# Performance work log

Measured on AMD Instinct MI355X. Metric: run time of the kernel, lower is better.

The kernel has to match this reference:

```python
import jax, jax.numpy as jnp
import numpy as np

N_U, N_P, E, E_LAB = 100000, 50000, 2000000, 500000
D_U, D_P, H = 64, 128, 64


def _seg_mean(feat, idx, n):
    # scatter-mean: sum per destination / clamp(count, 1)
    s = jax.ops.segment_sum(feat, idx, num_segments=n)
    c = jax.ops.segment_sum(jnp.ones((idx.shape[0],), feat.dtype), idx, num_segments=n)
    return s / jnp.maximum(c, 1.0)[:, None]


def setup_inputs() -> dict:
    key = jax.random.key(0)
    ks = jax.random.split(key, 16)
    inp = {
        'x_user': jax.random.normal(ks[0], (N_U, D_U), jnp.float32),
        'x_product': jax.random.normal(ks[1], (N_P, D_P), jnp.float32),
        'W1_buys_l': jax.random.normal(ks[2], (D_U, H), jnp.float32) * 0.05,
        'b1_buys': jnp.zeros((H,), jnp.float32),
        'W1_buys_r': jax.random.normal(ks[3], (D_P, H), jnp.float32) * 0.05,
        'W1_rev_l': jax.random.normal(ks[4], (D_P, H), jnp.float32) * 0.05,
        'b1_rev': jnp.zeros((H,), jnp.float32),
        'W1_rev_r': jax.random.normal(ks[5], (D_U, H), jnp.float32) * 0.05,
        'W2_buys_l': jax.random.normal(ks[6], (H, H), jnp.float32) * 0.05,
        'b2_buys': jnp.zeros((H,), jnp.float32),
        'W2_buys_r': jax.random.normal(ks[7], (H, H), jnp.float32) * 0.05,
        'W2_rev_l': jax.random.normal(ks[8], (H, H), jnp.float32) * 0.05,
        'b2_rev': jnp.zeros((H,), jnp.float32),
        'W2_rev_r': jax.random.normal(ks[9], (H, H), jnp.float32) * 0.05,
        'edge_src': jax.random.randint(ks[10], (E,), 0, N_U, jnp.int32),
        'edge_dst': jax.random.randint(ks[11], (E,), 0, N_P, jnp.int32),
        'lab_u': jax.random.randint(ks[12], (E_LAB,), 0, N_U, jnp.int32),
        'lab_p': jax.random.randint(ks[13], (E_LAB,), 0, N_P, jnp.int32),
    }
    return inp


def reference(x_user, x_product, W1_buys_l, b1_buys, W1_buys_r, W1_rev_l, b1_rev, W1_rev_r,
              W2_buys_l, b2_buys, W2_buys_r, W2_rev_l, b2_rev, W2_rev_r,
              edge_src, edge_dst, lab_u, lab_p):
    # SAGEConv (mean aggr): out_dst = mean_agg(x_src) @ W_l + b + x_dst @ W_r
    def sage(x_src, x_dst, src, dst, n_dst, Wl, b, Wr):
        agg = _seg_mean(x_src[src], dst, n_dst)
        return agg @ Wl + b + x_dst @ Wr

    n_u, n_p = x_user.shape[0], x_product.shape[0]
    # layer 1 (per edge type, hetero) + relu
    h_p = jax.nn.relu(sage(x_user, x_product, edge_src, edge_dst, n_p, W1_buys_l, b1_buys, W1_buys_r))
    h_u = jax.nn.relu(sage(x_product, x_user, edge_dst, edge_src, n_u, W1_rev_l, b1_rev, W1_rev_r))
    # layer 2
    h_p2 = sage(h_u, h_p, edge_src, edge_dst, n_p, W2_buys_l, b2_buys, W2_buys_r)
    h_u2 = sage(h_p, h_u, edge_dst, edge_src, n_u, W2_rev_l, b2_rev, W2_rev_r)
    # classifier: per-label-edge dot product
    return jnp.sum(h_u2[lab_u] * h_p2[lab_p], axis=-1)
```

## Files before the change

kernel.cpp:

```cpp
#include <hip/hip_runtime.h>


using u16 = unsigned short;
using u32 = unsigned int;

__device__ __forceinline__ u16 bf16r(float f) {
    u32 b = __float_as_uint(f);
    b += 0x7fffu + ((b >> 16) & 1u);
    return (u16)(b >> 16);
}
__device__ __forceinline__ float bflo(u32 u) { return __uint_as_float(u << 16); }
__device__ __forceinline__ float bfhi(u32 u) { return __uint_as_float(u & 0xffff0000u); }

#define BSH 8
#define MAXB 512
#define CHUNK 4096
#define RPT 16

__global__ __launch_bounds__(256) void k_histA(const int* __restrict__ esrc,
                                               const int* __restrict__ edst,
                                               int* __restrict__ bcntP,
                                               int* __restrict__ bcntU,
                                               int NBP, int NBU, int E) {
    __shared__ int hP[MAXB];
    __shared__ int hU[MAXB];
    int tid = threadIdx.x;
    for (int i = tid; i < MAXB; i += 256) { hP[i] = 0; hU[i] = 0; }
    __syncthreads();
    int E4 = E >> 2;
    const int4* s4 = (const int4*)esrc;
    const int4* d4 = (const int4*)edst;
    int stride = gridDim.x * 256;
    for (int i = blockIdx.x * 256 + tid; i < E4; i += stride) {
        int4 s = s4[i], d = d4[i];
        atomicAdd(&hU[s.x >> BSH], 1); atomicAdd(&hU[s.y >> BSH], 1);
        atomicAdd(&hU[s.z >> BSH], 1); atomicAdd(&hU[s.w >> BSH], 1);
        atomicAdd(&hP[d.x >> BSH], 1); atomicAdd(&hP[d.y >> BSH], 1);
        atomicAdd(&hP[d.z >> BSH], 1); atomicAdd(&hP[d.w >> BSH], 1);
    }
    if (blockIdx.x == 0 && tid < (E & 3)) {
        int e = E4 * 4 + tid;
        atomicAdd(&hU[esrc[e] >> BSH], 1);
        atomicAdd(&hP[edst[e] >> BSH], 1);
    }
    __syncthreads();
    for (int i = tid; i < NBP; i += 256) if (hP[i]) atomicAdd(&bcntP[i], hP[i]);
    for (int i = tid; i < NBU; i += 256) if (hU[i]) atomicAdd(&bcntU[i], hU[i]);
}

__global__ __launch_bounds__(256) void k_scanBuckets(const int* __restrict__ cntP,
                                                     int* __restrict__ basesP,
                                                     int* __restrict__ curP, int NBP,
                                                     const int* __restrict__ cntU,
                                                     int* __restrict__ basesU,
                                                     int* __restrict__ curU, int NBU) {
    const int* cnt; int* bases; int* cur; int NB;
    if (blockIdx.x == 0) { cnt = cntP; bases = basesP; cur = curP; NB = NBP; }
    else                 { cnt = cntU; bases = basesU; cur = curU; NB = NBU; }
    __shared__ int sA[MAXB];
    __shared__ int sB[MAXB];
    int tid = threadIdx.x;
    int v0 = (tid < NB) ? cnt[tid] : 0;
    int v1 = (tid + 256 < NB) ? cnt[tid + 256] : 0;
    sA[tid] = v0; sA[tid + 256] = v1;
    __syncthreads();
    int* src = sA; int* dst = sB;
    for (int off = 1; off < MAXB; off <<= 1) {
        dst[tid] = src[tid] + ((tid >= off) ? src[tid - off] : 0);
        int i2 = tid + 256;
        dst[i2] = src[i2] + ((i2 >= off) ? src[i2 - off] : 0);
        __syncthreads();
        int* t = src; src = dst; dst = t;
    }
    if (tid < NB)       { bases[tid] = src[tid] - v0;             cur[tid] = src[tid] - v0; }
    if (tid + 256 < NB) { bases[tid + 256] = src[tid + 256] - v1; cur[tid + 256] = src[tid + 256] - v1; }
    if (tid == 0) bases[NB] = src[MAXB - 1];
}

__global__ __launch_bounds__(256) void k_partition(const int* __restrict__ keys,
                                                   const int* __restrict__ payload,
                                                   int* __restrict__ cursor,
                                                   uint2* __restrict__ pairs,
                                                   int NB, int E) {
    __shared__ int hist[MAXB];
    __shared__ int sA[MAXB];
    __shared__ int sB[MAXB];
    __shared__ int bx[MAXB];
    __shared__ int gbase[MAXB];
    __shared__ uint2 prs[CHUNK];
    int tid = threadIdx.x;
    int i0 = blockIdx.x * CHUNK;
    int count = min(CHUNK, E - i0);
    for (int i = tid; i < MAXB; i += 256) hist[i] = 0;
    __syncthreads();
    int keyr[RPT], payr[RPT], rankr[RPT];
#pragma unroll
    for (int r = 0; r < RPT; ++r) {
        int idx = r * 256 + tid;
        if (idx < count) {
            int k = keys[i0 + idx];
            keyr[r] = k;
            payr[r] = payload[i0 + idx];
            rankr[r] = atomicAdd(&hist[k >> BSH], 1);
        } else keyr[r] = -1;
    }
    __syncthreads();
    sA[tid] = hist[tid]; sA[tid + 256] = hist[tid + 256];
    __syncthreads();
    int* src = sA; int* dst = sB;
    for (int off = 1; off < MAXB; off <<= 1) {
        dst[tid] = src[tid] + ((tid >= off) ? src[tid - off] : 0);
        int i2 = tid + 256;
        dst[i2] = src[i2] + ((i2 >= off) ? src[i2 - off] : 0);
        __syncthreads();
        int* t = src; src = dst; dst = t;
    }
    bx[tid] = src[tid] - hist[tid];
    bx[tid + 256] = src[tid + 256] - hist[tid + 256];
    __syncthreads();
    for (int b = tid; b < NB; b += 256) {
        int c = hist[b];
        gbase[b] = c ? atomicAdd(&cursor[b], c) : 0;
    }
#pragma unroll
    for (int r = 0; r < RPT; ++r) {
        if (keyr[r] >= 0)
            prs[bx[keyr[r] >> BSH] + rankr[r]] = make_uint2((u32)keyr[r], (u32)payr[r]);
    }
    __syncthreads();
    for (int j = tid; j < count; j += 256) {
        uint2 pr = prs[j];
        int b = pr.x >> BSH;
        pairs[gbase[b] + (j - bx[b])] = pr;
    }
}

__global__ __launch_bounds__(256) void k_bucketFill(
    const uint2* __restrict__ pairsP, const int* __restrict__ basesP, int NBP,
    int* __restrict__ nbr_p, int* __restrict__ deg_p, int* __restrict__ ptr_p, int NP,
    const uint2* __restrict__ pairsU, const int* __restrict__ basesU, int NBU,
    int* __restrict__ nbr_u, int* __restrict__ deg_u, int* __restrict__ ptr_u, int NU) {
    const uint2* pairs; const int* bases; int* nbr; int* deg; int* ptr; int N; int bucket;
    if ((int)blockIdx.x < NBP) {
        pairs = pairsP; bases = basesP; nbr = nbr_p; deg = deg_p; ptr = ptr_p; N = NP;
        bucket = blockIdx.x;
    } else {
        pairs = pairsU; bases = basesU; nbr = nbr_u; deg = deg_u; ptr = ptr_u; N = NU;
        bucket = blockIdx.x - NBP;
    }
    int tid = threadIdx.x;
    int base = bases[bucket];
    int cnt = bases[bucket + 1] - base;
    __shared__ int h[256];
    __shared__ int s[256];
    __shared__ int cur[256];
    h[tid] = 0;
    __syncthreads();
    for (int j = tid; j < cnt; j += 256) atomicAdd(&h[pairs[base + j].x & 255], 1);
    __syncthreads();
    int d = h[tid];
    s[tid] = d;
    __syncthreads();
    for (int off = 1; off < 256; off <<= 1) {
        int v = (tid >= off) ? s[tid - off] : 0;
        __syncthreads();
        s[tid] += v;
        __syncthreads();
    }
    int excl = s[tid] - d;
    int node = bucket * 256 + tid;
    if (node < N) { deg[node] = d; ptr[node] = base + excl; }
    cur[tid] = excl;
    __syncthreads();
    for (int j = tid; j < cnt; j += 256) {
        uint2 pr = pairs[base + j];
        int pos = atomicAdd(&cur[pr.x & 255], 1);
        nbr[base + pos] = pr.y;
    }
}

__global__ __launch_bounds__(256) void k_cast8(const float* __restrict__ x,
                                               u16* __restrict__ y, int n8) {
    int i = blockIdx.x * 256 + threadIdx.x;
    if (i >= n8) return;
    const float4* x4 = (const float4*)x;
    float4 a = x4[i * 2], b = x4[i * 2 + 1];
    uint4 o;
    o.x = (u32)bf16r(a.x) | ((u32)bf16r(a.y) << 16);
    o.y = (u32)bf16r(a.z) | ((u32)bf16r(a.w) << 16);
    o.z = (u32)bf16r(b.x) | ((u32)bf16r(b.y) << 16);
    o.w = (u32)bf16r(b.z) | ((u32)bf16r(b.w) << 16);
    ((uint4*)y)[i] = o;
}

__global__ __launch_bounds__(256) void k_transform_bf128(const float* __restrict__ x,
                                                         const float* __restrict__ W,
                                                         u16* __restrict__ ybf, int N) {
    __shared__ float Ws[128 * 64];
    __shared__ float xs[4][128];
    const int tid = threadIdx.x;
    for (int i = tid; i < 128 * 64; i += 256) Ws[i] = W[i];
    const int r = tid >> 6, c = tid & 63;
    const int row0 = blockIdx.x * 4;
    for (int i = tid; i < 4 * 128; i += 256) {
        int rr = i >> 7, kk = i & 127;
        int row = row0 + rr;
        xs[rr][kk] = (row < N) ? x[row * 128 + kk] : 0.f;
    }
    __syncthreads();
    const int row = row0 + r;
    if (row >= N) return;
    float acc = 0.f;
#pragma unroll 8
    for (int k = 0; k < 128; ++k) acc += xs[r][k] * Ws[k * 64 + c];
    ybf[row * 64 + c] = bf16r(acc);
}

__global__ __launch_bounds__(256) void k_gather2(
    const u16* __restrict__ yA, const int* __restrict__ nbrA, const int* __restrict__ startA,
    const int* __restrict__ degA, float* __restrict__ aggA, int NA,
    const u16* __restrict__ yB, const int* __restrict__ nbrB, const int* __restrict__ startB,
    const int* __restrict__ degB, float* __restrict__ aggB, int NB) {
    int w = (blockIdx.x * 256 + threadIdx.x) >> 6;
    int lane = threadIdx.x & 63;
    if (w >= NA + NB) return;
    const u16* y; const int* nbr; const int* stp; const int* deg; float* agg; int n;
    if (w < NA) { y = yA; nbr = nbrA; stp = startA; deg = degA; agg = aggA; n = w; }
    else        { y = yB; nbr = nbrB; stp = startB; deg = degB; agg = aggB; n = w - NA; }
    const int q = lane >> 3, t = lane & 7;
    const int d = deg[n];
    int j = stp[n];
    const int end = j + d;
    float a0=0,a1=0,a2=0,a3=0,a4=0,a5=0,a6=0,a7=0;
    float b0=0,b1=0,b2=0,b3=0,b4=0,b5=0,b6=0,b7=0;
    for (; j + 16 <= end; j += 16) {
        int g0 = nbr[j + q], g1 = nbr[j + 8 + q];
        uint4 v0 = *(const uint4*)(y + g0 * 64 + t * 8);
        uint4 v1 = *(const uint4*)(y + g1 * 64 + t * 8);
        a0 += bflo(v0.x); a1 += bfhi(v0.x); a2 += bflo(v0.y); a3 += bfhi(v0.y);
        a4 += bflo(v0.z); a5 += bfhi(v0.z); a6 += bflo(v0.w); a7 += bfhi(v0.w);
        b0 += bflo(v1.x); b1 += bfhi(v1.x); b2 += bflo(v1.y); b3 += bfhi(v1.y);
        b4 += bflo(v1.z); b5 += bfhi(v1.z); b6 += bflo(v1.w); b7 += bfhi(v1.w);
    }
    for (; j + 8 <= end; j += 8) {
        int g0 = nbr[j + q];
        uint4 v0 = *(const uint4*)(y + g0 * 64 + t * 8);
        a0 += bflo(v0.x); a1 += bfhi(v0.x); a2 += bflo(v0.y); a3 += bfhi(v0.y);
        a4 += bflo(v0.z); a5 += bfhi(v0.z); a6 += bflo(v0.w); a7 += bfhi(v0.w);
    }
    if (j + q < end) {
        int g0 = nbr[j + q];
        uint4 v0 = *(const uint4*)(y + g0 * 64 + t * 8);
        a0 += bflo(v0.x); a1 += bfhi(v0.x); a2 += bflo(v0.y); a3 += bfhi(v0.y);
        a4 += bflo(v0.z); a5 += bfhi(v0.z); a6 += bflo(v0.w); a7 += bfhi(v0.w);
    }
    a0 += b0; a1 += b1; a2 += b2; a3 += b3; a4 += b4; a5 += b5; a6 += b6; a7 += b7;
#pragma unroll
    for (int m = 8; m < 64; m <<= 1) {
        a0 += __shfl_xor(a0, m, 64); a1 += __shfl_xor(a1, m, 64);
        a2 += __shfl_xor(a2, m, 64); a3 += __shfl_xor(a3, m, 64);
        a4 += __shfl_xor(a4, m, 64); a5 += __shfl_xor(a5, m, 64);
        a6 += __shfl_xor(a6, m, 64); a7 += __shfl_xor(a7, m, 64);
    }
    if (q == 0) {
        float dinv = 1.0f / (float)max(d, 1);
        float* dstp = agg + n * 64 + t * 8;
        float4 o0, o1;
        o0.x = a0 * dinv; o0.y = a1 * dinv; o0.z = a2 * dinv; o0.w = a3 * dinv;
        o1.x = a4 * dinv; o1.y = a5 * dinv; o1.z = a6 * dinv; o1.w = a7 * dinv;
        *(float4*)dstp = o0;
        *(float4*)(dstp + 4) = o1;
    }
}

#define FMA_ROW(ACC, O, W4) \
    ACC[0] += (O) * (W4).x; ACC[1] += (O) * (W4).y; \
    ACC[2] += (O) * (W4).z; ACC[3] += (O) * (W4).w;

template <int K, int ROWS, bool RELU, bool EMIT, bool PRE, bool BIAS>
__global__ __launch_bounds__(256) void k_ctile(const float* __restrict__ pre,
                                               const float* __restrict__ bias,
                                               const float* __restrict__ x,
                                               const float* __restrict__ W,
                                               float* __restrict__ h,
                                               u16* __restrict__ hbf, int N) {
    constexpr int RR = ROWS / 16;
    constexpr int STRIDE = K + 4;
    constexpr int KF4 = K / 4;
    __shared__ float Ws[K * 64];
    __shared__ float op[ROWS * STRIDE];
    const int tid = threadIdx.x;
    for (int i = tid; i < K * 16; i += 256)
        ((float4*)Ws)[i] = ((const float4*)W)[i];
    const int c4 = (tid & 15) * 4;
    const int rb = (tid >> 4) * RR;
    float bx_ = 0.f, by_ = 0.f, bz_ = 0.f, bw_ = 0.f;
    if (BIAS) {
        float4 b4 = *(const float4*)(bias + c4);
        bx_ = b4.x; by_ = b4.y; bz_ = b4.z; bw_ = b4.w;
    }
    const int ntiles = (N + ROWS - 1) / ROWS;
    for (int tile = blockIdx.x; tile < ntiles; tile += gridDim.x) {
        const int row0 = tile * ROWS;
        __syncthreads();
        for (int i = tid; i < ROWS * KF4; i += 256) {
            int r = i / KF4, k4 = (i % KF4) * 4;
            int row = row0 + r;
            float4 v = make_float4(0.f, 0.f, 0.f, 0.f);
            if (row < N) v = *(const float4*)(x + (size_t)row * K + k4);
            *(float4*)(op + r * STRIDE + k4) = v;
        }
        __syncthreads();
        float acc[RR][4];
#pragma unroll
        for (int i = 0; i < RR; ++i) {
            float px = 0.f, py = 0.f, pz = 0.f, pw = 0.f;
            if (PRE) {
                int row = row0 + rb + i;
                if (row < N) {
                    float4 p = *(const float4*)(pre + row * 64 + c4);
                    px = p.x; py = p.y; pz = p.z; pw = p.w;
                }
            }
            acc[i][0] = bx_ + px; acc[i][1] = by_ + py;
            acc[i][2] = bz_ + pz; acc[i][3] = bw_ + pw;
        }
        for (int kk = 0; kk < K; kk += 4) {
            float4 w0 = *(const float4*)(Ws + (kk + 0) * 64 + c4);
            float4 w1 = *(const float4*)(Ws + (kk + 1) * 64 + c4);
            float4 w2 = *(const float4*)(Ws + (kk + 2) * 64 + c4);
            float4 w3 = *(const float4*)(Ws + (kk + 3) * 64 + c4);
#pragma unroll
            for (int i = 0; i < RR; ++i) {
                float4 o = *(const float4*)(op + (rb + i) * STRIDE + kk);
                FMA_ROW(acc[i], o.x, w0);
                FMA_ROW(acc[i], o.y, w1);
                FMA_ROW(acc[i], o.z, w2);
                FMA_ROW(acc[i], o.w, w3);
            }
        }
#pragma unroll
        for (int i = 0; i < RR; ++i) {
            int row = row0 + rb + i;
            if (row >= N) continue;
            float v0 = acc[i][0], v1 = acc[i][1], v2 = acc[i][2], v3 = acc[i][3];
            if (RELU) {
                v0 = fmaxf(v0, 0.f); v1 = fmaxf(v1, 0.f);
                v2 = fmaxf(v2, 0.f); v3 = fmaxf(v3, 0.f);
            }
            *(float4*)(h + row * 64 + c4) = make_float4(v0, v1, v2, v3);
            if (EMIT) {
                uint2 o;
                o.x = (u32)bf16r(v0) | ((u32)bf16r(v1) << 16);
                o.y = (u32)bf16r(v2) | ((u32)bf16r(v3) << 16);
                *(uint2*)(hbf + row * 64 + c4) = o;
            }
        }
    }
}

__global__ __launch_bounds__(256) void k_classify4(const float* __restrict__ hu,
                                                   const float* __restrict__ hp,
                                                   const int* __restrict__ lu,
                                                   const int* __restrict__ lp,
                                                   float* __restrict__ out, int EL) {
    int w = (blockIdx.x * 256 + threadIdx.x) >> 6;
    int lane = threadIdx.x & 63;
    int q = lane >> 4, t = lane & 15;
    int e = w * 4 + q;
    float v = 0.f;
    if (e < EL) {
        int u = lu[e], p = lp[e];
        float4 a = *(const float4*)(hu + u * 64 + t * 4);
        float4 b = *(const float4*)(hp + p * 64 + t * 4);
        v = a.x * b.x + a.y * b.y + a.z * b.z + a.w * b.w;
    }
#pragma unroll
    for (int m = 1; m < 16; m <<= 1) v += __shfl_xor(v, m, 64);
    if (t == 0 && e < EL) out[e] = v;
}

extern "C" void kernel_launch(void* const* d_in, const int* in_sizes, int n_in,
                              void* d_out, int out_size, void* d_ws, size_t ws_size,
                              hipStream_t stream) {
    const float* x_user    = (const float*)d_in[0];
    const float* x_product = (const float*)d_in[1];
    const float* W1bl = (const float*)d_in[2];
    const float* b1b  = (const float*)d_in[3];
    const float* W1br = (const float*)d_in[4];
    const float* W1rl = (const float*)d_in[5];
    const float* b1r  = (const float*)d_in[6];
    const float* W1rr = (const float*)d_in[7];
    const float* W2bl = (const float*)d_in[8];
    const float* b2b  = (const float*)d_in[9];
    const float* W2br = (const float*)d_in[10];
    const float* W2rl = (const float*)d_in[11];
    const float* b2r  = (const float*)d_in[12];
    const float* W2rr = (const float*)d_in[13];
    const int* esrc = (const int*)d_in[14];
    const int* edst = (const int*)d_in[15];
    const int* lu   = (const int*)d_in[16];
    const int* lp   = (const int*)d_in[17];

    const int NU = in_sizes[0] / 64;
    const int NP = in_sizes[1] / 128;
    const int E  = in_sizes[14];
    const int EL = in_sizes[16];
    const int NBP = (NP + 255) >> BSH;
    const int NBU = (NU + 255) >> BSH;

    char* ws = (char*)d_ws;
    size_t off = 0;
    auto alloc = [&](size_t bytes) -> void* {
        void* p = ws + off;
        off += (bytes + 255) & ~(size_t)255;
        return p;
    };
    int*   deg_u  = (int*)alloc((size_t)NU * 4);
    int*   deg_p  = (int*)alloc((size_t)NP * 4);
    int*   ptr_u  = (int*)alloc((size_t)NU * 4);
    int*   ptr_p  = (int*)alloc((size_t)NP * 4);
    int*   bcntP  = (int*)alloc((size_t)MAXB * 4);
    int*   bcntU  = (int*)alloc((size_t)MAXB * 4);
    int*   basesP = (int*)alloc((size_t)(MAXB + 1) * 4);
    int*   basesU = (int*)alloc((size_t)(MAXB + 1) * 4);
    int*   curP   = (int*)alloc((size_t)MAXB * 4);
    int*   curU   = (int*)alloc((size_t)MAXB * 4);
    int*   nbr_u  = (int*)alloc((size_t)E * 4);
    int*   nbr_p  = (int*)alloc((size_t)E * 4);
    size_t aggBytes = (size_t)(NP + NU) * 64 * 4;
    size_t pairBytes = (size_t)E * 8 * 2;
    char* uni = (char*)alloc(aggBytes > pairBytes ? aggBytes : pairBytes);
    float* aggP   = (float*)uni;
    float* aggU   = (float*)(uni + (size_t)NP * 64 * 4);
    uint2* pairsP = (uint2*)uni;
    uint2* pairsU = (uint2*)(uni + (size_t)E * 8);
    u16*   bfA    = (u16*)alloc((size_t)NU * 64 * 2);
    u16*   bfB    = (u16*)alloc((size_t)NP * 64 * 2);
    float* h_p    = (float*)alloc((size_t)NP * 64 * 4);
    float* h_u    = (float*)alloc((size_t)NU * 64 * 4);

    hipMemsetAsync(bcntP, 0, (size_t)MAXB * 2 * 4, stream);
    k_histA<<<512, 256, 0, stream>>>(esrc, edst, bcntP, bcntU, NBP, NBU, E);
    k_scanBuckets<<<2, 256, 0, stream>>>(bcntP, basesP, curP, NBP, bcntU, basesU, curU, NBU);
    const int pblocks = (E + CHUNK - 1) / CHUNK;
    k_partition<<<pblocks, 256, 0, stream>>>(edst, esrc, curP, pairsP, NBP, E);
    k_partition<<<pblocks, 256, 0, stream>>>(esrc, edst, curU, pairsU, NBU, E);
    k_bucketFill<<<NBP + NBU, 256, 0, stream>>>(pairsP, basesP, NBP, nbr_p, deg_p, ptr_p, NP,
                                                pairsU, basesU, NBU, nbr_u, deg_u, ptr_u, NU);

    k_cast8<<<(NU * 64 / 8 + 255) / 256, 256, 0, stream>>>(x_user, bfA, NU * 64 / 8);
    k_transform_bf128<<<(NP + 3) / 4, 256, 0, stream>>>(x_product, W1rl, bfB, NP);

    const int tP64 = (NP + 63) / 64, tU64 = (NU + 63) / 64, tP32 = (NP + 31) / 32;
    auto cap = [](int t, int c) { return t < c ? t : c; };

    k_gather2<<<(NP + NU + 3) / 4, 256, 0, stream>>>(bfA, nbr_p, ptr_p, deg_p, aggP, NP,
                                                     bfB, nbr_u, ptr_u, deg_u, aggU, NU);
    k_ctile<64, 64, false, false, false, true><<<cap(tP64, 1024), 256, 0, stream>>>(
        nullptr, b1b, aggP, W1bl, h_p, nullptr, NP);
    k_ctile<128, 32, true, true, true, false><<<cap(tP32, 768), 256, 0, stream>>>(
        h_p, nullptr, x_product, W1br, h_p, bfB, NP);
    k_ctile<64, 64, true, true, true, true><<<cap(tU64, 1024), 256, 0, stream>>>(
        aggU, b1r, x_user, W1rr, h_u, bfA, NU);

    k_gather2<<<(NP + NU + 3) / 4, 256, 0, stream>>>(bfA, nbr_p, ptr_p, deg_p, aggP, NP,
                                                     bfB, nbr_u, ptr_u, deg_u, aggU, NU);
    k_ctile<64, 64, false, false, false, true><<<cap(tP64, 1024), 256, 0, stream>>>(
        nullptr, b2b, aggP, W2bl, aggP, nullptr, NP);
    k_ctile<64, 64, false, false, false, true><<<cap(tU64, 1024), 256, 0, stream>>>(
        nullptr, b2r, aggU, W2rl, aggU, nullptr, NU);
    k_ctile<64, 64, false, false, true, false><<<cap(tP64, 1024), 256, 0, stream>>>(
        aggP, nullptr, h_p, W2br, h_p, nullptr, NP);
    k_ctile<64, 64, false, false, true, false><<<cap(tU64, 1024), 256, 0, stream>>>(
        aggU, nullptr, h_u, W2rr, h_u, nullptr, NU);

    k_classify4<<<((EL + 3) / 4 + 3) / 4, 256, 0, stream>>>(h_u, h_p, lu, lp, (float*)d_out, EL);
}
```

Before: 574.9 us.

## Fuse dual-input SAGE matmuls into one kernel and split combined gather

Adds k_ctile2, which computes agg@Wl + x@Wr + bias in one pass with both weight matrices in dynamic LDS. This replaces the pairs of k_ctile launches that round-tripped intermediates through global memory. The product-side layer-1 transform now reuses a k_ctile variant with a STORE=false template flag instead of a dedicated kernel. The merged two-graph gather is split into two separate k_gather1 launches. Fusing removes intermediate reads and writes and some launches, at the cost of larger LDS per block, which may reduce occupancy. Layer 2 writes h_p and h_u in place, and this stays safe only because each tile stages its rows into LDS before writing them back.

```diff
diff --git a/kernel.cpp b/kernel.cpp
--- a/kernel.cpp
+++ b/kernel.cpp
@@ -193,42 +193,16 @@
     ((uint4*)y)[i] = o;
 }
 
-__global__ __launch_bounds__(256) void k_transform_bf128(const float* __restrict__ x,
-                                                         const float* __restrict__ W,
-                                                         u16* __restrict__ ybf, int N) {
-    __shared__ float Ws[128 * 64];
-    __shared__ float xs[4][128];
-    const int tid = threadIdx.x;
-    for (int i = tid; i < 128 * 64; i += 256) Ws[i] = W[i];
-    const int r = tid >> 6, c = tid & 63;
-    const int row0 = blockIdx.x * 4;
-    for (int i = tid; i < 4 * 128; i += 256) {
-        int rr = i >> 7, kk = i & 127;
-        int row = row0 + rr;
-        xs[rr][kk] = (row < N) ? x[row * 128 + kk] : 0.f;
-    }
-    __syncthreads();
-    const int row = row0 + r;
-    if (row >= N) return;
-    float acc = 0.f;
-#pragma unroll 8
-    for (int k = 0; k < 128; ++k) acc += xs[r][k] * Ws[k * 64 + c];
-    ybf[row * 64 + c] = bf16r(acc);
-}
-
-__global__ __launch_bounds__(256) void k_gather2(
-    const u16* __restrict__ yA, const int* __restrict__ nbrA, const int* __restrict__ startA,
-    const int* __restrict__ degA, float* __restrict__ aggA, int NA,
-    const u16* __restrict__ yB, const int* __restrict__ nbrB, const int* __restrict__ startB,
-    const int* __restrict__ degB, float* __restrict__ aggB, int NB) {
-    int w = (blockIdx.x * 256 + threadIdx.x) >> 6;
+__global__ __launch_bounds__(256) void k_gather1(const u16* __restrict__ y,
+                                                 const int* __restrict__ nbr,
+                                                 const int* __restrict__ stp,
+                                                 const int* __restrict__ degp,
+                                                 float* __restrict__ agg, int N) {
+    int n = (blockIdx.x * 256 + threadIdx.x) >> 6;
     int lane = threadIdx.x & 63;
-    if (w >= NA + NB) return;
-    const u16* y; const int* nbr; const int* stp; const int* deg; float* agg; int n;
-    if (w < NA) { y = yA; nbr = nbrA; stp = startA; deg = degA; agg = aggA; n = w; }
-    else        { y = yB; nbr = nbrB; stp = startB; deg = degB; agg = aggB; n = w - NA; }
+    if (n >= N) return;
     const int q = lane >> 3, t = lane & 7;
-    const int d = deg[n];
+    const int d = degp[n];
     int j = stp[n];
     const int end = j + d;
     float a0=0,a1=0,a2=0,a3=0,a4=0,a5=0,a6=0,a7=0;
@@ -265,11 +239,8 @@
     if (q == 0) {
         float dinv = 1.0f / (float)max(d, 1);
         float* dstp = agg + n * 64 + t * 8;
-        float4 o0, o1;
-        o0.x = a0 * dinv; o0.y = a1 * dinv; o0.z = a2 * dinv; o0.w = a3 * dinv;
-        o1.x = a4 * dinv; o1.y = a5 * dinv; o1.z = a6 * dinv; o1.w = a7 * dinv;
-        *(float4*)dstp = o0;
-        *(float4*)(dstp + 4) = o1;
+        *(float4*)dstp       = make_float4(a0 * dinv, a1 * dinv, a2 * dinv, a3 * dinv);
+        *(float4*)(dstp + 4) = make_float4(a4 * dinv, a5 * dinv, a6 * dinv, a7 * dinv);
     }
 }
 
@@ -277,7 +248,7 @@
     ACC[0] += (O) * (W4).x; ACC[1] += (O) * (W4).y; \
     ACC[2] += (O) * (W4).z; ACC[3] += (O) * (W4).w;
 
-template <int K, int ROWS, bool RELU, bool EMIT, bool PRE, bool BIAS>
+template <int K, int ROWS, bool RELU, bool EMIT, bool PRE, bool BIAS, bool STORE>
 __global__ __launch_bounds__(256) void k_ctile(const float* __restrict__ pre,
                                                const float* __restrict__ bias,
                                                const float* __restrict__ x,
@@ -333,6 +304,104 @@
 #pragma unroll
             for (int i = 0; i < RR; ++i) {
                 float4 o = *(const float4*)(op + (rb + i) * STRIDE + kk);
+                FMA_ROW(acc[i], o.x, w0);
+                FMA_ROW(acc[i], o.y, w1);
+                FMA_ROW(acc[i], o.z, w2);
+                FMA_ROW(acc[i], o.w, w3);
+            }
+        }
+#pragma unroll
+        for (int i = 0; i < RR; ++i) {
+            int row = row0 + rb + i;
+            if (row >= N) continue;
+            float v0 = acc[i][0], v1 = acc[i][1], v2 = acc[i][2], v3 = acc[i][3];
+            if (RELU) {
+                v0 = fmaxf(v0, 0.f); v1 = fmaxf(v1, 0.f);
+                v2 = fmaxf(v2, 0.f); v3 = fmaxf(v3, 0.f);
+            }
+            if (STORE)
+                *(float4*)(h + row * 64 + c4) = make_float4(v0, v1, v2, v3);
+            if (EMIT) {
+                uint2 o;
+                o.x = (u32)bf16r(v0) | ((u32)bf16r(v1) << 16);
+                o.y = (u32)bf16r(v2) | ((u32)bf16r(v3) << 16);
+                *(uint2*)(hbf + row * 64 + c4) = o;
+            }
+        }
+    }
+}
+
+template <int K1, int K2, bool RELU, bool EMIT, bool BIAS>
+__global__ __launch_bounds__(256) void k_ctile2(const float* __restrict__ x1,
+                                                const float* __restrict__ x2,
+                                                const float* __restrict__ W1,
+                                                const float* __restrict__ W2,
+                                                const float* __restrict__ bias,
+                                                float* __restrict__ h,
+                                                u16* __restrict__ hbf, int N) {
+    constexpr int ROWS = 32, RR = 2;
+    constexpr int S1 = K1 + 4, S2 = K2 + 4;
+    extern __shared__ float sm[];
+    float* Ws1 = sm;
+    float* Ws2 = Ws1 + K1 * 64;
+    float* op1 = Ws2 + K2 * 64;
+    float* op2 = op1 + ROWS * S1;
+    const int tid = threadIdx.x;
+    for (int i = tid; i < K1 * 16; i += 256) ((float4*)Ws1)[i] = ((const float4*)W1)[i];
+    for (int i = tid; i < K2 * 16; i += 256) ((float4*)Ws2)[i] = ((const float4*)W2)[i];
+    const int c4 = (tid & 15) * 4;
+    const int rb = (tid >> 4) * RR;
+    float bx_ = 0.f, by_ = 0.f, bz_ = 0.f, bw_ = 0.f;
+    if (BIAS) {
+        float4 b4 = *(const float4*)(bias + c4);
+        bx_ = b4.x; by_ = b4.y; bz_ = b4.z; bw_ = b4.w;
+    }
+    const int ntiles = (N + ROWS - 1) / ROWS;
+    for (int tile = blockIdx.x; tile < ntiles; tile += gridDim.x) {
+        const int row0 = tile * ROWS;
+        __syncthreads();
+        for (int i = tid; i < ROWS * (K1 / 4); i += 256) {
+            int r = i / (K1 / 4), k4 = (i % (K1 / 4)) * 4;
+            int row = row0 + r;
+            float4 v = make_float4(0.f, 0.f, 0.f, 0.f);
+            if (row < N) v = *(const float4*)(x1 + (size_t)row * K1 + k4);
+            *(float4*)(op1 + r * S1 + k4) = v;
+        }
+        for (int i = tid; i < ROWS * (K2 / 4); i += 256) {
+            int r = i / (K2 / 4), k4 = (i % (K2 / 4)) * 4;
+            int row = row0 + r;
+            float4 v = make_float4(0.f, 0.f, 0.f, 0.f);
+            if (row < N) v = *(const float4*)(x2 + (size_t)row * K2 + k4);
+            *(float4*)(op2 + r * S2 + k4) = v;
+        }
+        __syncthreads();
+        float acc[RR][4];
+#pragma unroll
+        for (int i = 0; i < RR; ++i) {
+            acc[i][0] = bx_; acc[i][1] = by_; acc[i][2] = bz_; acc[i][3] = bw_;
+        }
+        for (int kk = 0; kk < K1; kk += 4) {
+            float4 w0 = *(const float4*)(Ws1 + (kk + 0) * 64 + c4);
+            float4 w1 = *(const float4*)(Ws1 + (kk + 1) * 64 + c4);
+            float4 w2 = *(const float4*)(Ws1 + (kk + 2) * 64 + c4);
+            float4 w3 = *(const float4*)(Ws1 + (kk + 3) * 64 + c4);
+#pragma unroll
+            for (int i = 0; i < RR; ++i) {
+                float4 o = *(const float4*)(op1 + (rb + i) * S1 + kk);
+                FMA_ROW(acc[i], o.x, w0);
+                FMA_ROW(acc[i], o.y, w1);
+                FMA_ROW(acc[i], o.z, w2);
+                FMA_ROW(acc[i], o.w, w3);
+            }
+        }
+        for (int kk = 0; kk < K2; kk += 4) {
+            float4 w0 = *(const float4*)(Ws2 + (kk + 0) * 64 + c4);
+            float4 w1 = *(const float4*)(Ws2 + (kk + 1) * 64 + c4);
+            float4 w2 = *(const float4*)(Ws2 + (kk + 2) * 64 + c4);
+            float4 w3 = *(const float4*)(Ws2 + (kk + 3) * 64 + c4);
+#pragma unroll
+            for (int i = 0; i < RR; ++i) {
+                float4 o = *(const float4*)(op2 + (rb + i) * S2 + kk);
                 FMA_ROW(acc[i], o.x, w0);
                 FMA_ROW(acc[i], o.y, w1);
                 FMA_ROW(acc[i], o.z, w2);
@@ -450,30 +519,30 @@
                                                 pairsU, basesU, NBU, nbr_u, deg_u, ptr_u, NU);
 
     k_cast8<<<(NU * 64 / 8 + 255) / 256, 256, 0, stream>>>(x_user, bfA, NU * 64 / 8);
-    k_transform_bf128<<<(NP + 3) / 4, 256, 0, stream>>>(x_product, W1rl, bfB, NP);
-
-    const int tP64 = (NP + 63) / 64, tU64 = (NU + 63) / 64, tP32 = (NP + 31) / 32;
+    {
+        const int tiles = (NP + 31) / 32;
+        k_ctile<128, 32, false, true, false, false, false><<<(tiles < 768 ? tiles : 768), 256, 0, stream>>>(
+            nullptr, nullptr, x_product, W1rl, nullptr, bfB, NP);
+    }
+
+    const size_t ldsL1b = ((64 + 128) * 64 + 32 * (64 + 4) + 32 * (128 + 4)) * sizeof(float);
+    const size_t ldsL2  = ((64 + 64) * 64 + 2 * 32 * (64 + 4)) * sizeof(float);
+    const int tP32 = (NP + 31) / 32, tU32 = (NU + 31) / 32, tU64 = (NU + 63) / 64;
     auto cap = [](int t, int c) { return t < c ? t : c; };
 
-    k_gather2<<<(NP + NU + 3) / 4, 256, 0, stream>>>(bfA, nbr_p, ptr_p, deg_p, aggP, NP,
-                                                     bfB, nbr_u, ptr_u, deg_u, aggU, NU);
-    k_ctile<64, 64, false, false, false, true><<<cap(tP64, 1024), 256, 0, stream>>>(
-        nullptr, b1b, aggP, W1bl, h_p, nullptr, NP);
-    k_ctile<128, 32, true, true, true, false><<<cap(tP32, 768), 256, 0, stream>>>(
-        h_p, nullptr, x_product, W1br, h_p, bfB, NP);
-    k_ctile<64, 64, true, true, true, true><<<cap(tU64, 1024), 256, 0, stream>>>(
+    k_gather1<<<(NP + 3) / 4, 256, 0, stream>>>(bfA, nbr_p, ptr_p, deg_p, aggP, NP);
+    k_gather1<<<(NU + 3) / 4, 256, 0, stream>>>(bfB, nbr_u, ptr_u, deg_u, aggU, NU);
+    k_ctile2<64, 128, true, true, true><<<cap(tP32, 512), 256, ldsL1b, stream>>>(
+        aggP, x_product, W1bl, W1br, b1b, h_p, bfB, NP);
+    k_ctile<64, 64, true, true, true, true, true><<<cap(tU64, 1024), 256, 0, stream>>>(
         aggU, b1r, x_user, W1rr, h_u, bfA, NU);
 
-    k_gather2<<<(NP + NU + 3) / 4, 256, 0, stream>>>(bfA, nbr_p, ptr_p, deg_p, aggP, NP,
-                                                     bfB, nbr_u, ptr_u, deg_u, aggU, NU);
-    k_ctile<64, 64, false, false, false, true><<<cap(tP64, 1024), 256, 0, stream>>>(
-        nullptr, b2b, aggP, W2bl, aggP, nullptr, NP);
-    k_ctile<64, 64, false, false, false, true><<<cap(tU64, 1024), 256, 0, stream>>>(
-        nullptr, b2r, aggU, W2rl, aggU, nullptr, NU);
-    k_ctile<64, 64, false, false, true, false><<<cap(tP64, 1024), 256, 0, stream>>>(
-        aggP, nullptr, h_p, W2br, h_p, nullptr, NP);
-    k_ctile<64, 64, false, false, true, false><<<cap(tU64, 1024), 256, 0, stream>>>(
-        aggU, nullptr, h_u, W2rr, h_u, nullptr, NU);
+    k_gather1<<<(NP + 3) / 4, 256, 0, stream>>>(bfA, nbr_p, ptr_p, deg_p, aggP, NP);
+    k_gather1<<<(NU + 3) / 4, 256, 0, stream>>>(bfB, nbr_u, ptr_u, deg_u, aggU, NU);
+    k_ctile2<64, 64, false, false, true><<<cap(tP32, 768), 256, ldsL2, stream>>>(
+        aggP, h_p, W2bl, W2br, b2b, h_p, nullptr, NP);
+    k_ctile2<64, 64, false, false, true><<<cap(tU32, 768), 256, ldsL2, stream>>>(
+        aggU, h_u, W2rl, W2rr, b2r, h_u, nullptr, NU);
 
     k_classify4<<<((EL + 3) / 4 + 3) / 4, 256, 0, stream>>>(h_u, h_p, lu, lp, (float*)d_out, EL);
 }
```

Result: slower. 1.083 ms (+88.4%).
